# Performance work log

Measured on AMD Instinct MI355X. Metric: run time of the kernel, lower is better.

Reference implementation:

```python
import jax, jax.numpy as jnp
import numpy as np

B, N, C, H = 2, 2048, 768, 12
HD = C // H  # head dim = 64


def setup_inputs() -> dict:
    key = jax.random.key(0)
    k1, k2, k3 = jax.random.split(key, 3)
    x = jax.random.normal(k1, (B, N, C), dtype=jnp.float32)
    w_qkv = jax.random.normal(k2, (C, 3 * C), dtype=jnp.float32) * (C ** -0.5)
    w_proj = jax.random.normal(k3, (C, C), dtype=jnp.float32) * (C ** -0.5)
    b_proj = jnp.zeros((C,), dtype=jnp.float32)
    return {"x": x, "w_qkv": w_qkv, "w_proj": w_proj, "b_proj": b_proj}


def reference(x, w_qkv, w_proj, b_proj):
    scale = HD ** -0.5
    # qkv projection: [B,N,3C] -> [3,B,H,N,HD]
    qkv = (x @ w_qkv).reshape(B, N, 3, H, HD).transpose(2, 0, 3, 1, 4)
    q, k, v = qkv[0], qkv[1], qkv[2]
    # explicit QK^T softmax V (materializes [B,H,N,N] scores, as in source)
    attn = jnp.einsum("bhqd,bhkd->bhqk", q, k) * scale
    attn = jax.nn.softmax(attn, axis=-1)
    out = jnp.einsum("bhqk,bhkd->bhqd", attn, v)
    out = out.transpose(0, 2, 1, 3).reshape(B, N, C)
    return out @ w_proj + b_proj
```

## Files before the change

kernel.cpp:

```cpp
#include <hip/hip_runtime.h>

#define C_DIM 768
#define NSEQ 2048
#define H_DIM 12
#define HD 64
#define M_ROWS 4096
#define KSPLIT 2

typedef float f32x4 __attribute__((ext_vector_type(4)));
typedef short bf16x8 __attribute__((ext_vector_type(8)));
typedef _Float16 f16x8 __attribute__((ext_vector_type(8)));
typedef _Float16 f16x4 __attribute__((ext_vector_type(4)));
typedef __fp16 fp16x2 __attribute__((ext_vector_type(2)));
typedef __fp16 fp16x4 __attribute__((ext_vector_type(4)));
typedef unsigned short u16;

#define MFMA_PV(a, b, c) __builtin_amdgcn_mfma_f32_16x16x16f16(a, b, c, 0, 0, 0)

typedef unsigned int __attribute__((address_space(1))) as1_uint;
typedef unsigned int __attribute__((address_space(3))) as3_uint;
__device__ __forceinline__ void dma16(const void* g, void* l) {
  __builtin_amdgcn_global_load_lds((const as1_uint*)g, (as3_uint*)l, 16, 0, 0);
}

__device__ __forceinline__ u16 f2bf(float f) {
  union { float f; unsigned u; } v; v.f = f;
  unsigned u = v.u + 0x7FFFu + ((v.u >> 16) & 1u);
  return (u16)(u >> 16);
}

__global__ __launch_bounds__(256) void cvt_x_kernel(const float* __restrict__ in,
                                                    u16* __restrict__ out, int n4) {
  int i = blockIdx.x * 256 + threadIdx.x;
  if (i < n4) {
    float4 v = ((const float4*)in)[i];
    ushort4 o;
    o.x = f2bf(v.x); o.y = f2bf(v.y); o.z = f2bf(v.z); o.w = f2bf(v.w);
    ((ushort4*)out)[i] = o;
  }
}

__global__ __launch_bounds__(256) void transpose_cvt_kernel(const float* __restrict__ wq,
                                                            const float* __restrict__ wp,
                                                            u16* __restrict__ outq,
                                                            u16* __restrict__ outp) {
  const float* in; u16* out; int Cc;
  if (blockIdx.z == 0) { in = wq; out = outq; Cc = 3 * C_DIM; }
  else { if (blockIdx.x >= 24) return; in = wp; out = outp; Cc = C_DIM; }
  const int R = C_DIM;
  __shared__ float t[32][33];
  int tx = threadIdx.x & 31, ty = threadIdx.x >> 5;
  int c0 = blockIdx.x * 32, r0 = blockIdx.y * 32;
#pragma unroll
  for (int i = 0; i < 4; i++)
    t[ty + i * 8][tx] = in[(size_t)(r0 + ty + i * 8) * Cc + c0 + tx];
  __syncthreads();
#pragma unroll
  for (int i = 0; i < 4; i++)
    out[(size_t)(c0 + ty + i * 8) * R + r0 + tx] = f2bf(t[tx][ty + i * 8]);
}

__device__ __forceinline__ void gemm_core_128(const u16* __restrict__ A,
                                              const u16* __restrict__ BT,
                                              int m0, int n0,
                                              u16* la, u16* lb, f32x4 acc[4][4]) {
  const int K = C_DIM;
  int tid = threadIdx.x, lane = tid & 63, wave = tid >> 6;
  int wm = (wave >> 1) * 64, wn = (wave & 1) * 64;
  int quad = lane >> 4, l16 = lane & 15;

  int r0 = wave * 16 + (lane >> 2);
  int sw = (((lane & 3) ^ (r0 & 3)) * 8);
  const u16* ga0 = A + (size_t)(m0 + r0) * K + sw;
  const u16* ga1 = A + (size_t)(m0 + r0 + 64) * K + sw;
  const u16* gb0 = BT + (size_t)(n0 + r0) * K + sw;
  const u16* gb1 = BT + (size_t)(n0 + r0 + 64) * K + sw;
  u16* lA0 = la + wave * 16 * 32;
  u16* lA1 = lA0 + 64 * 32;
  u16* lB0 = lb + wave * 16 * 32;
  u16* lB1 = lB0 + 64 * 32;

  for (int k0 = 0; k0 < K; k0 += 32) {
    __syncthreads();
    dma16(ga0 + k0, lA0);
    dma16(ga1 + k0, lA1);
    dma16(gb0 + k0, lB0);
    dma16(gb1 + k0, lB1);
    __syncthreads();
    bf16x8 af[4], bfr[4];
#pragma unroll
    for (int mt = 0; mt < 4; mt++) {
      int r = wm + mt * 16 + l16;
      af[mt] = *(const bf16x8*)(la + r * 32 + ((quad ^ (r & 3)) * 8));
    }
#pragma unroll
    for (int nt = 0; nt < 4; nt++) {
      int r = wn + nt * 16 + l16;
      bfr[nt] = *(const bf16x8*)(lb + r * 32 + ((quad ^ (r & 3)) * 8));
    }
#pragma unroll
    for (int mt = 0; mt < 4; mt++)
#pragma unroll
      for (int nt = 0; nt < 4; nt++)
        acc[mt][nt] = __builtin_amdgcn_mfma_f32_16x16x32_bf16(af[mt], bfr[nt], acc[mt][nt], 0, 0, 0);
  }
}

__device__ __forceinline__ void gemm_core_64(const u16* __restrict__ A,
                                             const u16* __restrict__ BT,
                                             int m0, int n0,
                                             u16* la, u16* lb, f32x4 acc[2][4]) {
  const int K = C_DIM;
  int tid = threadIdx.x, lane = tid & 63, wave = tid >> 6;
  int wm = (wave >> 1) * 32, wn = (wave & 1) * 64;
  int quad = lane >> 4, l16 = lane & 15;

  int r0 = wave * 16 + (lane >> 2);
  int sw = (((lane & 3) ^ (r0 & 3)) * 8);
  const u16* ga0 = A + (size_t)(m0 + r0) * K + sw;
  const u16* gb0 = BT + (size_t)(n0 + r0) * K + sw;
  const u16* gb1 = BT + (size_t)(n0 + r0 + 64) * K + sw;
  u16* lA0 = la + wave * 16 * 32;
  u16* lB0 = lb + wave * 16 * 32;
  u16* lB1 = lB0 + 64 * 32;

  for (int k0 = 0; k0 < K; k0 += 32) {
    __syncthreads();
    dma16(ga0 + k0, lA0);
    dma16(gb0 + k0, lB0);
    dma16(gb1 + k0, lB1);
    __syncthreads();
    bf16x8 af[2], bfr[4];
#pragma unroll
    for (int mt = 0; mt < 2; mt++) {
      int r = wm + mt * 16 + l16;
      af[mt] = *(const bf16x8*)(la + r * 32 + ((quad ^ (r & 3)) * 8));
    }
#pragma unroll
    for (int nt = 0; nt < 4; nt++) {
      int r = wn + nt * 16 + l16;
      bfr[nt] = *(const bf16x8*)(lb + r * 32 + ((quad ^ (r & 3)) * 8));
    }
#pragma unroll
    for (int mt = 0; mt < 2; mt++)
#pragma unroll
      for (int nt = 0; nt < 4; nt++)
        acc[mt][nt] = __builtin_amdgcn_mfma_f32_16x16x32_bf16(af[mt], bfr[nt], acc[mt][nt], 0, 0, 0);
  }
}

#define Q_PRESCALE 0.18033688011112042f
__global__ __launch_bounds__(256) void gemm_qkv_kernel(const u16* __restrict__ A,
                                                       const u16* __restrict__ BT,
                                                       _Float16* __restrict__ qb,
                                                       _Float16* __restrict__ kb,
                                                       _Float16* __restrict__ vtb) {
  __shared__ __align__(16) u16 la[128 * 32];
  __shared__ __align__(16) u16 lb[128 * 32];
  f32x4 acc[4][4] = {};
  int m0 = blockIdx.x * 128, n0 = blockIdx.y * 128;
  gemm_core_128(A, BT, m0, n0, la, lb, acc);

  int lane = threadIdx.x & 63, wave = threadIdx.x >> 6;
  int wm = (wave >> 1) * 64, wn = (wave & 1) * 64;
  int quad = lane >> 4, l16 = lane & 15;
#pragma unroll
  for (int mt = 0; mt < 4; mt++) {
#pragma unroll
    for (int nt = 0; nt < 4; nt++) {
      int gn = n0 + wn + nt * 16 + l16;
      int which = gn / C_DIM;
      int cc = gn - which * C_DIM;
      int h = cc >> 6, d = cc & 63;
      int gm0 = m0 + wm + mt * 16 + quad * 4;
      int b = gm0 >> 11, n = gm0 & 2047;
      size_t bh = (size_t)(b * H_DIM + h);
      if (which == 2) {
        f16x4 hv;
#pragma unroll
        for (int r = 0; r < 4; r++) hv[r] = (_Float16)acc[mt][nt][r];
        *(f16x4*)(vtb + (bh * HD + d) * NSEQ + n) = hv;
      } else if (which == 0) {
#pragma unroll
        for (int r = 0; r < 4; r++)
          qb[(bh * NSEQ + n + r) * HD + d] = (_Float16)(acc[mt][nt][r] * Q_PRESCALE);
      } else {
#pragma unroll
        for (int r = 0; r < 4; r++)
          kb[(bh * NSEQ + n + r) * HD + d] = (_Float16)acc[mt][nt][r];
      }
    }
  }
}

__global__ __launch_bounds__(256) void gemm_proj_kernel(const u16* __restrict__ A,
                                                        const u16* __restrict__ BT,
                                                        const float* __restrict__ bias,
                                                        float* __restrict__ out) {
  __shared__ __align__(16) u16 la[64 * 32];
  __shared__ __align__(16) u16 lb[128 * 32];
  f32x4 acc[2][4] = {};
  int m0 = blockIdx.x * 64, n0 = blockIdx.y * 128;
  gemm_core_64(A, BT, m0, n0, la, lb, acc);

  int lane = threadIdx.x & 63, wave = threadIdx.x >> 6;
  int wm = (wave >> 1) * 32, wn = (wave & 1) * 64;
  int quad = lane >> 4, l16 = lane & 15;
#pragma unroll
  for (int mt = 0; mt < 2; mt++) {
#pragma unroll
    for (int nt = 0; nt < 4; nt++) {
      int gn = n0 + wn + nt * 16 + l16;
      float bv = bias[gn];
#pragma unroll
      for (int r = 0; r < 4; r++) {
        int gm = m0 + wm + mt * 16 + quad * 4 + r;
        out[(size_t)gm * C_DIM + gn] = acc[mt][nt][r] + bv;
      }
    }
  }
}

__global__ __launch_bounds__(256) void attn_kernel(const _Float16* __restrict__ qb,
                                                   const _Float16* __restrict__ kb,
                                                   const _Float16* __restrict__ vtb,
                                                   __fp16* __restrict__ opart,
                                                   float* __restrict__ lpart) {
  __shared__ __align__(16) u16 lk[2][64 * 72];
  __shared__ __align__(16) u16 lv[2][64 * 72];
  int bh = blockIdx.y, qblk = blockIdx.x, ks = blockIdx.z;
  int tid = threadIdx.x, lane = tid & 63, wave = tid >> 6;
  int quad = lane >> 4, l16 = lane & 15;

  const _Float16* q_bh = qb + (size_t)bh * NSEQ * HD;
  const u16* k_bh = (const u16*)(kb + (size_t)bh * NSEQ * HD);
  const u16* v_bh = (const u16*)(vtb + (size_t)bh * HD * NSEQ);

  int q0 = qblk * 128 + wave * 32 + l16;
  f16x8 qf[2][2];
#pragma unroll
  for (int qt = 0; qt < 2; qt++) {
    const _Float16* qp = q_bh + (size_t)(q0 + qt * 16) * HD + quad * 8;
    qf[qt][0] = *(const f16x8*)qp;
    qf[qt][1] = *(const f16x8*)(qp + 32);
  }

  f32x4 o[2][4] = {};
  float l_i[2] = {0.f, 0.f};

  int srow = tid >> 3, scj = tid & 7;
  const u16* kp0 = k_bh + (size_t)srow * HD + scj * 8;
  const u16* kp1 = kp0 + (size_t)32 * HD;
  const u16* vp0 = v_bh + (size_t)srow * NSEQ + scj * 8;
  const u16* vp1 = vp0 + (size_t)32 * NSEQ;
  int w0 = srow * 72 + scj * 8, w1 = (srow + 32) * 72 + scj * 8;

  const int kt_beg = ks * (NSEQ / 64 / KSPLIT);
  const int kt_end = kt_beg + (NSEQ / 64 / KSPLIT);

  {
    int k0 = kt_beg * 64;
    *(uint4*)(lk[0] + w0) = *(const uint4*)(kp0 + (size_t)k0 * HD);
    *(uint4*)(lk[0] + w1) = *(const uint4*)(kp1 + (size_t)k0 * HD);
    *(uint4*)(lv[0] + w0) = *(const uint4*)(vp0 + k0);
    *(uint4*)(lv[0] + w1) = *(const uint4*)(vp1 + k0);
  }

  for (int kt = kt_beg; kt < kt_end; kt++) {
    int cur = kt & 1, nxt = cur ^ 1;
    __syncthreads();

    uint4 rk0, rk1, rv0, rv1;
    if (kt < kt_end - 1) {
      int k0 = (kt + 1) * 64;
      rk0 = *(const uint4*)(kp0 + (size_t)k0 * HD);
      rk1 = *(const uint4*)(kp1 + (size_t)k0 * HD);
      rv0 = *(const uint4*)(vp0 + k0);
      rv1 = *(const uint4*)(vp1 + k0);
    }

    f32x4 s0[4], s1[4];
#pragma unroll
    for (int nt = 0; nt < 4; nt++) {
      const u16* kp = lk[cur] + (nt * 16 + l16) * 72 + quad * 8;
      f16x8 kf0 = *(const f16x8*)kp;
      f16x8 kf1 = *(const f16x8*)(kp + 32);
      f32x4 t0 = {}, t1 = {};
      t0 = __builtin_amdgcn_mfma_f32_16x16x32_f16(kf0, qf[0][0], t0, 0, 0, 0);
      t0 = __builtin_amdgcn_mfma_f32_16x16x32_f16(kf1, qf[0][1], t0, 0, 0, 0);
      t1 = __builtin_amdgcn_mfma_f32_16x16x32_f16(kf0, qf[1][0], t1, 0, 0, 0);
      t1 = __builtin_amdgcn_mfma_f32_16x16x32_f16(kf1, qf[1][1], t1, 0, 0, 0);
      s0[nt] = t0; s1[nt] = t1;
    }

#pragma unroll
    for (int nt = 0; nt < 4; nt++) {
      float a0 = __builtin_amdgcn_exp2f(s0[nt][0]);
      float a1 = __builtin_amdgcn_exp2f(s0[nt][1]);
      float a2 = __builtin_amdgcn_exp2f(s0[nt][2]);
      float a3 = __builtin_amdgcn_exp2f(s0[nt][3]);
      l_i[0] += (a0 + a1) + (a2 + a3);
      float b0 = __builtin_amdgcn_exp2f(s1[nt][0]);
      float b1 = __builtin_amdgcn_exp2f(s1[nt][1]);
      float b2 = __builtin_amdgcn_exp2f(s1[nt][2]);
      float b3 = __builtin_amdgcn_exp2f(s1[nt][3]);
      l_i[1] += (b0 + b1) + (b2 + b3);
      union { fp16x2 h2[2]; f16x4 h4; } pa, pb;
      pa.h2[0] = __builtin_amdgcn_cvt_pkrtz(a0, a1);
      pa.h2[1] = __builtin_amdgcn_cvt_pkrtz(a2, a3);
      pb.h2[0] = __builtin_amdgcn_cvt_pkrtz(b0, b1);
      pb.h2[1] = __builtin_amdgcn_cvt_pkrtz(b2, b3);
#pragma unroll
      for (int dt = 0; dt < 4; dt++) {
        f16x4 vf = *(const f16x4*)(lv[cur] + (dt * 16 + l16) * 72 + nt * 16 + quad * 4);
        o[0][dt] = MFMA_PV(vf, pa.h4, o[0][dt]);
        o[1][dt] = MFMA_PV(vf, pb.h4, o[1][dt]);
      }
    }

    if (kt < kt_end - 1) {
      *(uint4*)(lk[nxt] + w0) = rk0;
      *(uint4*)(lk[nxt] + w1) = rk1;
      *(uint4*)(lv[nxt] + w0) = rv0;
      *(uint4*)(lv[nxt] + w1) = rv1;
    }
  }

#pragma unroll
  for (int qt = 0; qt < 2; qt++) {
    l_i[qt] += __shfl_xor(l_i[qt], 16);
    l_i[qt] += __shfl_xor(l_i[qt], 32);
  }

  int b = bh / H_DIM, h = bh % H_DIM;
  __fp16* obase = opart + (size_t)ks * M_ROWS * C_DIM;
  float* lrow = lpart + ((size_t)ks * H_DIM * 2 + bh) * NSEQ;
#pragma unroll
  for (int qt = 0; qt < 2; qt++) {
    int q = q0 + qt * 16;
    if (quad == 0) lrow[q] = l_i[qt];
    __fp16* orow = obase + (size_t)(b * NSEQ + q) * C_DIM + h * HD;
#pragma unroll
    for (int dt = 0; dt < 4; dt++) {
      union { fp16x2 h2[2]; fp16x4 h4; } ov;
      ov.h2[0] = __builtin_amdgcn_cvt_pkrtz(o[qt][dt][0], o[qt][dt][1]);
      ov.h2[1] = __builtin_amdgcn_cvt_pkrtz(o[qt][dt][2], o[qt][dt][3]);
      *(fp16x4*)(orow + dt * 16 + quad * 4) = ov.h4;
    }
  }
}

__global__ __launch_bounds__(256) void combine_kernel(const __fp16* __restrict__ opart,
                                                      const float* __restrict__ lpart,
                                                      u16* __restrict__ attn) {
  int idx = blockIdx.x * 256 + threadIdx.x;
  int bq = idx / (C_DIM / 8);
  int c = (idx - bq * (C_DIM / 8)) * 8;
  int h = c >> 6;
  int b = bq >> 11, q = bq & 2047;
  size_t lidx = (size_t)(b * H_DIM + h) * NSEQ + q;
  float l = lpart[lidx] + lpart[lidx + (size_t)H_DIM * 2 * NSEQ];
  float inv = 1.f / l;
  const __fp16* p0 = opart + (size_t)bq * C_DIM + c;
  const __fp16* p1 = p0 + (size_t)M_ROWS * C_DIM;
  fp16x4 a0 = *(const fp16x4*)p0, a1 = *(const fp16x4*)(p0 + 4);
  fp16x4 b0 = *(const fp16x4*)p1, b1 = *(const fp16x4*)(p1 + 4);
  union { ushort4 s4[2]; uint4 u4; } ov;
#pragma unroll
  for (int j = 0; j < 4; j++) {
    ov.s4[0].x = f2bf(((float)a0[0] + (float)b0[0]) * inv);
  }
  ov.s4[0].x = f2bf(((float)a0[0] + (float)b0[0]) * inv);
  ov.s4[0].y = f2bf(((float)a0[1] + (float)b0[1]) * inv);
  ov.s4[0].z = f2bf(((float)a0[2] + (float)b0[2]) * inv);
  ov.s4[0].w = f2bf(((float)a0[3] + (float)b0[3]) * inv);
  ov.s4[1].x = f2bf(((float)a1[0] + (float)b1[0]) * inv);
  ov.s4[1].y = f2bf(((float)a1[1] + (float)b1[1]) * inv);
  ov.s4[1].z = f2bf(((float)a1[2] + (float)b1[2]) * inv);
  ov.s4[1].w = f2bf(((float)a1[3] + (float)b1[3]) * inv);
  *(uint4*)(attn + (size_t)bq * C_DIM + c) = ov.u4;
}

extern "C" void kernel_launch(void* const* d_in, const int* in_sizes, int n_in,
                              void* d_out, int out_size, void* d_ws, size_t ws_size,
                              hipStream_t stream) {
  const float* x = (const float*)d_in[0];
  const float* w_qkv = (const float*)d_in[1];
  const float* w_proj = (const float*)d_in[2];
  const float* b_proj = (const float*)d_in[3];
  float* out = (float*)d_out;

  char* ws = (char*)d_ws;
  u16* x_bf        = (u16*)(ws);
  u16* wqkvT       = (u16*)(ws + 6291456);
  u16* wprojT      = (u16*)(ws + 9830400);
  _Float16* qb     = (_Float16*)(ws + 11010048);
  _Float16* kb     = (_Float16*)(ws + 17301504);
  _Float16* vtb    = (_Float16*)(ws + 23592960);
  __fp16* opart    = (__fp16*)(ws + 29884416);
  float* lpart     = (float*)(ws + 42467328);
  u16* attn        = x_bf;

  cvt_x_kernel<<<3072, 256, 0, stream>>>(x, x_bf, M_ROWS * C_DIM / 4);
  transpose_cvt_kernel<<<dim3(72, 24, 2), 256, 0, stream>>>(w_qkv, w_proj, wqkvT, wprojT);
  gemm_qkv_kernel<<<dim3(32, 18), 256, 0, stream>>>(x_bf, wqkvT, qb, kb, vtb);
  attn_kernel<<<dim3(16, 24, KSPLIT), 256, 0, stream>>>(qb, kb, vtb, opart, lpart);
  combine_kernel<<<M_ROWS * C_DIM / 8 / 256, 256, 0, stream>>>(opart, lpart, attn);
  gemm_proj_kernel<<<dim3(64, 6), 256, 0, stream>>>(attn, wprojT, b_proj, out);
}
```

Baseline: 159.9 us.

## Split attention keys four ways and fuse input conversion kernels into one launch

Raises the key-dimension split of the attention kernel from 2 to 4, which launches more workgroups to fill the GPU. The combine kernel now loops over all partial outputs and row sums, and the workspace layout is moved to fit the larger partial buffers. The x conversion and weight transpose/convert kernels are merged into a single launch to save one kernel launch. In exchange, the combine step reads twice as much partial data and each attention block does less work, which lowers reuse of its loaded tiles.

```diff
diff --git a/kernel.cpp b/kernel.cpp
--- a/kernel.cpp
+++ b/kernel.cpp
@@ -5,7 +5,7 @@
 #define H_DIM 12
 #define HD 64
 #define M_ROWS 4096
-#define KSPLIT 2
+#define KSPLIT 4
 
 typedef float f32x4 __attribute__((ext_vector_type(4)));
 typedef short bf16x8 __attribute__((ext_vector_type(8)));
@@ -29,21 +29,31 @@
   return (u16)(u >> 16);
 }
 
-__global__ __launch_bounds__(256) void cvt_x_kernel(const float* __restrict__ in,
-                                                    u16* __restrict__ out, int n4) {
-  int i = blockIdx.x * 256 + threadIdx.x;
-  if (i < n4) {
-    float4 v = ((const float4*)in)[i];
-    ushort4 o;
-    o.x = f2bf(v.x); o.y = f2bf(v.y); o.z = f2bf(v.z); o.w = f2bf(v.w);
-    ((ushort4*)out)[i] = o;
-  }
-}
-
-__global__ __launch_bounds__(256) void transpose_cvt_kernel(const float* __restrict__ wq,
-                                                            const float* __restrict__ wp,
-                                                            u16* __restrict__ outq,
-                                                            u16* __restrict__ outp) {
+__global__ __launch_bounds__(256) void prep_kernel(const float* __restrict__ x,
+                                                   const float* __restrict__ wq,
+                                                   const float* __restrict__ wp,
+                                                   u16* __restrict__ x_bf,
+                                                   u16* __restrict__ outq,
+                                                   u16* __restrict__ outp) {
+  if (blockIdx.z == 2) {
+    const int n4 = M_ROWS * C_DIM / 4;
+    int lb = blockIdx.y * 72 + blockIdx.x;
+    int i0 = lb * 256 + threadIdx.x;
+    {
+      float4 v = ((const float4*)x)[i0];
+      ushort4 o;
+      o.x = f2bf(v.x); o.y = f2bf(v.y); o.z = f2bf(v.z); o.w = f2bf(v.w);
+      ((ushort4*)x_bf)[i0] = o;
+    }
+    int i1 = i0 + 442368;
+    if (i1 < n4) {
+      float4 v = ((const float4*)x)[i1];
+      ushort4 o;
+      o.x = f2bf(v.x); o.y = f2bf(v.y); o.z = f2bf(v.z); o.w = f2bf(v.w);
+      ((ushort4*)x_bf)[i1] = o;
+    }
+    return;
+  }
   const float* in; u16* out; int Cc;
   if (blockIdx.z == 0) { in = wq; out = outq; Cc = 3 * C_DIM; }
   else { if (blockIdx.x >= 24) return; in = wp; out = outp; Cc = C_DIM; }
@@ -358,26 +368,27 @@
   int c = (idx - bq * (C_DIM / 8)) * 8;
   int h = c >> 6;
   int b = bq >> 11, q = bq & 2047;
-  size_t lidx = (size_t)(b * H_DIM + h) * NSEQ + q;
-  float l = lpart[lidx] + lpart[lidx + (size_t)H_DIM * 2 * NSEQ];
+  float l = 0.f;
+  float acc[8] = {0.f, 0.f, 0.f, 0.f, 0.f, 0.f, 0.f, 0.f};
+  const __fp16* p = opart + (size_t)bq * C_DIM + c;
+#pragma unroll
+  for (int ks = 0; ks < KSPLIT; ks++) {
+    l += lpart[((size_t)ks * H_DIM * 2 + b * H_DIM + h) * NSEQ + q];
+    fp16x4 a0 = *(const fp16x4*)(p + (size_t)ks * M_ROWS * C_DIM);
+    fp16x4 a1 = *(const fp16x4*)(p + (size_t)ks * M_ROWS * C_DIM + 4);
+#pragma unroll
+    for (int j = 0; j < 4; j++) { acc[j] += (float)a0[j]; acc[4 + j] += (float)a1[j]; }
+  }
   float inv = 1.f / l;
-  const __fp16* p0 = opart + (size_t)bq * C_DIM + c;
-  const __fp16* p1 = p0 + (size_t)M_ROWS * C_DIM;
-  fp16x4 a0 = *(const fp16x4*)p0, a1 = *(const fp16x4*)(p0 + 4);
-  fp16x4 b0 = *(const fp16x4*)p1, b1 = *(const fp16x4*)(p1 + 4);
   union { ushort4 s4[2]; uint4 u4; } ov;
-#pragma unroll
-  for (int j = 0; j < 4; j++) {
-    ov.s4[0].x = f2bf(((float)a0[0] + (float)b0[0]) * inv);
-  }
-  ov.s4[0].x = f2bf(((float)a0[0] + (float)b0[0]) * inv);
-  ov.s4[0].y = f2bf(((float)a0[1] + (float)b0[1]) * inv);
-  ov.s4[0].z = f2bf(((float)a0[2] + (float)b0[2]) * inv);
-  ov.s4[0].w = f2bf(((float)a0[3] + (float)b0[3]) * inv);
-  ov.s4[1].x = f2bf(((float)a1[0] + (float)b1[0]) * inv);
-  ov.s4[1].y = f2bf(((float)a1[1] + (float)b1[1]) * inv);
-  ov.s4[1].z = f2bf(((float)a1[2] + (float)b1[2]) * inv);
-  ov.s4[1].w = f2bf(((float)a1[3] + (float)b1[3]) * inv);
+  ov.s4[0].x = f2bf(acc[0] * inv);
+  ov.s4[0].y = f2bf(acc[1] * inv);
+  ov.s4[0].z = f2bf(acc[2] * inv);
+  ov.s4[0].w = f2bf(acc[3] * inv);
+  ov.s4[1].x = f2bf(acc[4] * inv);
+  ov.s4[1].y = f2bf(acc[5] * inv);
+  ov.s4[1].z = f2bf(acc[6] * inv);
+  ov.s4[1].w = f2bf(acc[7] * inv);
   *(uint4*)(attn + (size_t)bq * C_DIM + c) = ov.u4;
 }
 
@@ -398,11 +409,10 @@
   _Float16* kb     = (_Float16*)(ws + 17301504);
   _Float16* vtb    = (_Float16*)(ws + 23592960);
   __fp16* opart    = (__fp16*)(ws + 29884416);
-  float* lpart     = (float*)(ws + 42467328);
+  float* lpart     = (float*)(ws + 55050240);
   u16* attn        = x_bf;
 
-  cvt_x_kernel<<<3072, 256, 0, stream>>>(x, x_bf, M_ROWS * C_DIM / 4);
-  transpose_cvt_kernel<<<dim3(72, 24, 2), 256, 0, stream>>>(w_qkv, w_proj, wqkvT, wprojT);
+  prep_kernel<<<dim3(72, 24, 3), 256, 0, stream>>>(x, w_qkv, w_proj, x_bf, wqkvT, wprojT);
   gemm_qkv_kernel<<<dim3(32, 18), 256, 0, stream>>>(x_bf, wqkvT, qb, kb, vtb);
   attn_kernel<<<dim3(16, 24, KSPLIT), 256, 0, stream>>>(qb, kb, vtb, opart, lpart);
   combine_kernel<<<M_ROWS * C_DIM / 8 / 256, 256, 0, stream>>>(opart, lpart, attn);
```

Result: no change. 161.2 us (+0.8%).
